# Kernel optimization log

Hardware: AMD Instinct MI355X
Metric: run time of the kernel (lower is better)

Reference implementation:

```python
import jax, jax.numpy as jnp
import numpy as np

# ---- static configuration (matches init_kwargs / input_specs) ----
B, DIM, H, W = 2, 32, 512, 512
FOLD, P, HDIM, NCLS, CV = 8, 2, 96, 16, 96
S = P * P                      # superpixels per tile
h, w = H // FOLD, W // FOLD    # 64, 64 tile size
N = h * w                      # pixels per tile

# ---- static SSN neighbor tables (init label map -> 9 candidate spixels) ----
_lab = np.repeat(np.repeat(np.arange(S).reshape(P, P), h // P, 0), w // P, 1).reshape(-1)
_sy, _sx = _lab // P, _lab % P
_dy = np.repeat(np.array([-1, 0, 1]), 3)[:, None]
_dx = np.tile(np.array([-1, 0, 1]), 3)[:, None]
_ny, _nx = _sy[None] + _dy, _sx[None] + _dx
_valid = (_ny >= 0) & (_ny < P) & (_nx >= 0) & (_nx < P)
NBR = jnp.asarray(np.where(_valid, _ny * P + _nx, 0), dtype=jnp.int32)  # [9,N]
VALID = jnp.asarray(_valid)                                             # [9,N]

def _conv1x1(x, Wk, bk):
    return jnp.einsum('oc,bchw->bohw', Wk, x) + bk[None, :, None, None]

def _tiles(t):  # 'b c (f1 h) (f2 w) -> (b f1 f2) c h w'
    Bq, C = t.shape[:2]
    return t.reshape(Bq, C, FOLD, h, FOLD, w).transpose(0, 2, 4, 1, 3, 5).reshape(Bq * FOLD * FOLD, C, h, w)

def _pool(t):  # adaptive avg pool (h,w)->(P,P); returns [b,C,S]
    b, C = t.shape[:2]
    return t.reshape(b, C, P, h // P, P, w // P).mean((3, 5)).reshape(b, C, S)

def _affinity(Fp, cen):
    # Fp [b,Ctot,N], cen [b,Ctot,S]; squared-euclid dist pixel->9 neighbor spixels,
    # sparse softmax over the 9 candidates, then scatter to dense [b,S,N] affinity.
    d = (Fp * Fp).sum(1)[:, None, :] + (cen * cen).sum(1)[:, :, None] \
        - 2.0 * jnp.einsum('bcn,bcs->bsn', Fp, cen)          # [b,S,N]
    b = Fp.shape[0]
    idx = jnp.broadcast_to(NBR[None], (b, 9, N))
    d9 = jnp.where(VALID[None], jnp.take_along_axis(d, idx, axis=1), 1e16)
    aff = jax.nn.softmax(-d9, axis=1)                        # [b,9,N]
    bi = jnp.arange(b)[:, None, None]
    ni = jnp.arange(N)[None, None, :]
    return jnp.zeros((b, S, N), Fp.dtype).at[bi, idx, ni].add(jnp.where(VALID[None], aff, 0.0))

def setup_inputs():
    k = jax.random.split(jax.random.key(0), 6)
    return {
        'x': jax.random.normal(k[0], (B, DIM, H, W), jnp.float32),
        'feat': jax.random.normal(k[1], (B, CV, H, W), jnp.float32),
        'sdf_data': jax.random.normal(k[2], (B, DIM - 1, H, W), jnp.float32),
        'Wf': 0.1 * jax.random.normal(k[3], (HDIM, DIM), jnp.float32),
        'bf': jnp.zeros((HDIM,), jnp.float32),
        'Wsdf': 0.1 * jax.random.normal(k[4], (HDIM, DIM - 1), jnp.float32),
        'bsdf': jnp.zeros((HDIM,), jnp.float32),
        'gt': jax.random.randint(k[5], (B, H, W), 0, NCLS, jnp.int32),
    }

def _cluster(x, feat, sdf_data, Wf, bf, Wsdf, bsdf):
    hsi = _conv1x1(x, Wf, bf)
    sdf = _conv1x1(sdf_data, Wsdf, bsdf)
    pf = _tiles(feat).reshape(-1, CV, N)      # per-tile pixel (value) features
    df = _tiles(hsi).reshape(-1, HDIM, N)     # deep features
    sf = _tiles(sdf).reshape(-1, HDIM, N)     # sdf features
    b = pf.shape[0]
    cen_pf = _pool(pf.reshape(b, CV, h, w))
    cen_df = _pool(df.reshape(b, HDIM, h, w))
    cen_sf = _pool(sf.reshape(b, HDIM, h, w))
    value_centers = cen_pf.transpose(0, 2, 1)                # [b,S,C]
    Fall = jnp.concatenate([pf, df, sf], 1)
    # SSN iter 0: soft affinity, update pixel-feature centroids
    A0 = _affinity(Fall, jnp.concatenate([cen_pf, cen_df, cen_sf], 1))
    cen_pf = jnp.einsum('bsn,bcn->bcs', A0, pf) / (A0.sum(-1)[:, None, :] + 1e-16)
    # SSN iter 1 (last): final dense affinity; torch computes this under no_grad
    sim = jax.lax.stop_gradient(_affinity(Fall, jnp.concatenate([cen_pf, cen_df, cen_sf], 1)))
    mask = jax.nn.one_hot(jnp.argmax(sim, 1), S, axis=1, dtype=sim.dtype)   # hard argmax mask [b,S,N]
    sim = sim * mask
    out = (jnp.einsum('bsn,bnc->bsc', sim, pf.transpose(0, 2, 1)) + value_centers) \
          / (sim.sum(-1, keepdims=True) + 1.0)
    center_feat = out.reshape(B, FOLD * FOLD * S, CV)
    mask5 = mask.reshape(B, FOLD * FOLD, S, h, w)
    return center_feat, mask5

def _gen_labels(gt, mask5):
    T = FOLD * FOLD
    coef = jnp.arange(S, dtype=mask5.dtype).reshape(1, 1, S, 1, 1)
    small = (mask5 * coef).sum(2) + jnp.arange(0, T * S, S, dtype=mask5.dtype).reshape(1, T, 1, 1)
    spix_map = small.reshape(B, FOLD, FOLD, h, w).transpose(0, 1, 3, 2, 4).reshape(B, H, W)
    gt_r = gt.reshape(B, FOLD, h, FOLD, w).transpose(0, 1, 3, 2, 4).reshape(B, T, h, w) + 1
    gt_filt = (gt_r[:, :, None].astype(mask5.dtype) * mask5).reshape(B, T, S, N).astype(jnp.int32)
    count = jax.nn.one_hot(gt_filt, NCLS + 1, dtype=jnp.float32).sum(3)   # [B,T,S,NCLS+1]
    labels = count[..., 1:].transpose(0, 3, 1, 2).reshape(B, NCLS, T * S)
    return labels, spix_map

def reference(x, feat, sdf_data, Wf, bf, Wsdf, bsdf, gt):
    center_feat, mask5 = _cluster(x, feat, sdf_data, Wf, bf, Wsdf, bsdf)
    labels, spix_map = _gen_labels(gt, jax.lax.stop_gradient(mask5))
    return center_feat, labels, spix_map
```

## Files before the change

### kernel.cpp

```cpp
#include <hip/hip_runtime.h>
#include <hip/hip_bf16.h>


#define OFF_POOLX   0
#define OFF_POOLS   16384
#define OFF_CENPF0  32256
#define OFF_NUM1    114688
#define OFF_DEN1    163840
#define OFF_OUTNUM  214016
#define OFF_OUTDEN  263168
#define OFF_LABELS  263680
#define OFF_G       271872
#define ZERO_BASE   OFF_NUM1
#define ZERO_LEN    157184

#define OUT_CF 0
#define OUT_LB 49152
#define OUT_SP 57344

#define PL 262144

typedef float f32x4 __attribute__((ext_vector_type(4)));
typedef short bf16x8 __attribute__((ext_vector_type(8)));
typedef unsigned short u16x4 __attribute__((ext_vector_type(4)));

__device__ __forceinline__ unsigned short f2bf(float f) {
  return (unsigned short)(__float_as_uint(f) >> 16);
}

__global__ __launch_bounds__(256) void k_pool(const float* __restrict__ x,
    const float* __restrict__ feat, const float* __restrict__ sdf,
    float* __restrict__ ws) {
  int plane = blockIdx.x, f1 = blockIdx.y, tid = threadIdx.x;
  {
    int lb = blockIdx.y * gridDim.x + blockIdx.x;
    if (tid < 64) {
      int zi = lb * 64 + tid;
      if (zi < ZERO_LEN) ws[ZERO_BASE + zi] = 0.f;
    }
  }
  int b = plane / 159, ch = plane % 159;
  const float* src; int c, C, cls;
  if (ch < 32)      { src = x;    C = 32; c = ch;      cls = 0; }
  else if (ch < 63) { src = sdf;  C = 31; c = ch - 32; cls = 1; }
  else              { src = feat; C = 96; c = ch - 63; cls = 2; }
  const float* base = src + ((size_t)(b*C + c)*512 + f1*64)*512;
  int half = tid >> 7, col4 = tid & 127;
  const float* p0 = base + (size_t)half*512 + (size_t)col4*4;
  f32x4 v[16];
  float acc0 = 0.f, acc1 = 0.f;
  #pragma unroll
  for (int i = 0; i < 16; ++i)
    v[i] = *reinterpret_cast<const f32x4*>(p0 + (size_t)i*1024);
  #pragma unroll
  for (int i = 0; i < 16; ++i) { f32x4 t = v[i]; acc0 += t[0] + t[1] + t[2] + t[3]; }
  #pragma unroll
  for (int i = 0; i < 16; ++i)
    v[i] = *reinterpret_cast<const f32x4*>(p0 + (size_t)(16 + i)*1024);
  #pragma unroll
  for (int i = 0; i < 16; ++i) { f32x4 t = v[i]; acc1 += t[0] + t[1] + t[2] + t[3]; }
  acc0 += __shfl_xor(acc0, 1, 64); acc0 += __shfl_xor(acc0, 2, 64); acc0 += __shfl_xor(acc0, 4, 64);
  acc1 += __shfl_xor(acc1, 1, 64); acc1 += __shfl_xor(acc1, 2, 64); acc1 += __shfl_xor(acc1, 4, 64);
  __shared__ float part[32][2];
  int lane = tid & 63;
  if ((lane & 7) == 0) {
    int f2 = col4 >> 4, qx = (col4 >> 3) & 1;
    part[(f2*2 + qx)*2 + 0][half] = acc0;
    part[(f2*2 + qx)*2 + 1][half] = acc1;
  }
  __syncthreads();
  if (tid < 32) {
    float v2 = (part[tid][0] + part[tid][1]) * (1.f/1024.f);
    int f2 = tid >> 2, qx = (tid >> 1) & 1, qy = tid & 1;
    int tile = b*64 + f1*8 + f2, s = qy*2 + qx;
    float* dst;
    if (cls == 0)      dst = ws + OFF_POOLX  + (tile*32 + c)*4;
    else if (cls == 1) dst = ws + OFF_POOLS  + (tile*31 + c)*4;
    else               dst = ws + OFF_CENPF0 + (tile*96 + c)*4;
    dst[s] = v2;
  }
}

__global__ __launch_bounds__(256) void k_pass2(const float* __restrict__ x,
    const float* __restrict__ feat, const float* __restrict__ sdf,
    const float* __restrict__ Wf, const float* __restrict__ bfv,
    const float* __restrict__ Wsdf, const float* __restrict__ bsdf,
    float* __restrict__ ws) {
  int wg = blockIdx.x, tile = wg >> 2, seg = wg & 3, tid = threadIdx.x;
  int b = tile >> 6, tl = tile & 63, f1 = tl >> 3, f2 = tl & 7;
  __shared__ float s_cpf0[384];
  __shared__ float s_udf[128];
  __shared__ float s_usf[124];
  __shared__ float s_gc[4], s_n0[4];
  __shared__ __align__(16) unsigned short s_pfT[96][264];
  __shared__ __align__(16) unsigned short s_aT[16][264];
  __shared__ __align__(16) float s_part[2][8][260];
  float* scr  = reinterpret_cast<float*>(&s_pfT[0][0]);
  float* c_px = scr;
  float* c_ps = scr + 128;
  float* c_df = scr + 256;
  float* c_sf = scr + 640;
  for (int i = tid; i < 384; i += 256) s_cpf0[i] = ws[OFF_CENPF0 + tile*384 + i];
  if (tid < 128) c_px[tid] = ws[OFF_POOLX + tile*128 + tid];
  if (tid < 124) c_ps[tid] = ws[OFF_POOLS + tile*124 + tid];
  __syncthreads();
  for (int i = tid; i < 384; i += 256) {
    int c = i % 96, s = i / 96;
    float a = bfv[c];
    for (int k = 0; k < 32; ++k) a += Wf[c*32 + k] * c_px[k*4 + s];
    c_df[c*4 + s] = a;
    float a2 = bsdf[c];
    for (int k = 0; k < 31; ++k) a2 += Wsdf[c*31 + k] * c_ps[k*4 + s];
    c_sf[c*4 + s] = a2;
  }
  __syncthreads();
  if (tid < 128) {
    int s2 = tid >> 5, k = tid & 31;
    float u = 0.f;
    for (int c2 = 0; c2 < 96; ++c2) u += Wf[c2*32 + k] * c_df[c2*4 + s2];
    s_udf[tid] = u;
  } else if (tid < 252) {
    int t2 = tid - 128, s2 = t2 / 31, k = t2 % 31;
    float u = 0.f;
    for (int c2 = 0; c2 < 96; ++c2) u += Wsdf[c2*31 + k] * c_sf[c2*4 + s2];
    s_usf[t2] = u;
  } else {
    int s = tid - 252;
    float g = 0.f, n = 0.f;
    for (int c = 0; c < 96; ++c) {
      float a = c_df[c*4 + s], a2 = c_sf[c*4 + s];
      g += 2.f*(bfv[c]*a + bsdf[c]*a2) - (a*a + a2*a2);
      float cp = s_cpf0[c*4 + s];
      n += cp*cp;
    }
    s_gc[s] = g; s_n0[s] = n;
  }
  for (int i = tid; i < 16*264; i += 256) (&s_aT[0][0])[i] = 0;
  __syncthreads();
  int lane = tid & 63, wave = tid >> 6;
  int mrow = lane & 15, quad = lane >> 4;
  int q4 = lane * 4;
  f32x4 zero4 = {0.f, 0.f, 0.f, 0.f};
  f32x4 accC[6] = {zero4, zero4, zero4, zero4, zero4, zero4};
  float dden[4] = {0.f, 0.f, 0.f, 0.f};
  const float* xb = x   + (size_t)(b*32)*PL;
  const float* sb = sdf + (size_t)(b*31)*PL;
  const float* fb = feat+ (size_t)(b*96)*PL;
  for (int chunk = 0; chunk < 4; ++chunk) {
    int pq = seg*1024 + chunk*256 + q4;
    int goq = (f1*64 + (pq >> 6))*512 + f2*64 + (pq & 63);
    f32x4 dpd[4] = {zero4, zero4, zero4, zero4};
    f32x4 dpp[4] = {zero4, zero4, zero4, zero4};
    f32x4 vv[8];
    #pragma unroll
    for (int i = 0; i < 8; ++i)
      vv[i] = *reinterpret_cast<const f32x4*>(xb + (size_t)(wave + 4*i)*PL + goq);
    #pragma unroll
    for (int i = 0; i < 8; ++i) {
      int ch = wave + 4*i;
      #pragma unroll
      for (int s = 0; s < 4; ++s) dpd[s] += vv[i] * s_udf[s*32 + ch];
    }
    #pragma unroll
    for (int i = 0; i < 8; ++i)
      if (wave + 4*i < 31)
        vv[i] = *reinterpret_cast<const f32x4*>(sb + (size_t)(wave + 4*i)*PL + goq);
    #pragma unroll
    for (int i = 0; i < 8; ++i) {
      int ch = wave + 4*i;
      if (ch < 31) {
        #pragma unroll
        for (int s = 0; s < 4; ++s) dpd[s] += vv[i] * s_usf[s*31 + ch];
      }
    }
    #pragma unroll
    for (int r = 0; r < 3; ++r) {
      #pragma unroll
      for (int i = 0; i < 8; ++i)
        vv[i] = *reinterpret_cast<const f32x4*>(fb + (size_t)(wave + 4*(r*8 + i))*PL + goq);
      #pragma unroll
      for (int i = 0; i < 8; ++i) {
        int ch = wave + 4*(r*8 + i);
        u16x4 uu = { f2bf(vv[i][0]), f2bf(vv[i][1]), f2bf(vv[i][2]), f2bf(vv[i][3]) };
        *reinterpret_cast<u16x4*>(&s_pfT[ch][q4]) = uu;
        #pragma unroll
        for (int s = 0; s < 4; ++s) dpp[s] += vv[i] * s_cpf0[ch*4 + s];
      }
    }
    if (wave >= 2) {
      #pragma unroll
      for (int s = 0; s < 4; ++s) {
        *reinterpret_cast<f32x4*>(&s_part[wave-2][s][q4]) = dpd[s];
        *reinterpret_cast<f32x4*>(&s_part[wave-2][4+s][q4]) = dpp[s];
      }
    }
    __syncthreads();
    if (wave < 2) {
      #pragma unroll
      for (int s = 0; s < 4; ++s) {
        f32x4 t = *reinterpret_cast<f32x4*>(&s_part[wave][s][q4]);
        t += dpd[s];
        *reinterpret_cast<f32x4*>(&s_part[wave][s][q4]) = t;
        f32x4 t2 = *reinterpret_cast<f32x4*>(&s_part[wave][4+s][q4]);
        t2 += dpp[s];
        *reinterpret_cast<f32x4*>(&s_part[wave][4+s][q4]) = t2;
      }
    }
    __syncthreads();
    float d0 = s_part[0][0][tid] + s_part[1][0][tid];
    float d1 = s_part[0][1][tid] + s_part[1][1][tid];
    float d2 = s_part[0][2][tid] + s_part[1][2][tid];
    float d3 = s_part[0][3][tid] + s_part[1][3][tid];
    float p0 = s_part[0][4][tid] + s_part[1][4][tid];
    float p1 = s_part[0][5][tid] + s_part[1][5][tid];
    float p2 = s_part[0][6][tid] + s_part[1][6][tid];
    float p3 = s_part[0][7][tid] + s_part[1][7][tid];
    float g0 = 2.f*d0 + s_gc[0], g1 = 2.f*d1 + s_gc[1];
    float g2 = 2.f*d2 + s_gc[2], g3 = 2.f*d3 + s_gc[3];
    int p = seg*1024 + chunk*256 + tid;
    {
      f32x4 gv = {g0, g1, g2, g3};
      *reinterpret_cast<f32x4*>(ws + OFF_G + ((size_t)tile << 14) + (size_t)p*4) = gv;
    }
    float sc0 = g0 + 2.f*p0 - s_n0[0];
    float sc1 = g1 + 2.f*p1 - s_n0[1];
    float sc2 = g2 + 2.f*p2 - s_n0[2];
    float sc3 = g3 + 2.f*p3 - s_n0[3];
    float m = fmaxf(fmaxf(sc0, sc1), fmaxf(sc2, sc3));
    float e0 = expf(sc0 - m), e1 = expf(sc1 - m), e2 = expf(sc2 - m), e3 = expf(sc3 - m);
    float inv = 1.f / (e0 + e1 + e2 + e3);
    float a0 = e0*inv, a1 = e1*inv, a2 = e2*inv, a3 = e3*inv;
    s_aT[0][tid] = f2bf(a0); s_aT[1][tid] = f2bf(a1);
    s_aT[2][tid] = f2bf(a2); s_aT[3][tid] = f2bf(a3);
    dden[0] += a0; dden[1] += a1; dden[2] += a2; dden[3] += a3;
    __syncthreads();
    #pragma unroll
    for (int kk = 0; kk < 2; ++kk) {
      int k0 = (wave*2 + kk)*32 + quad*8;
      bf16x8 bfrag = *reinterpret_cast<const bf16x8*>(&s_aT[mrow][k0]);
      #pragma unroll
      for (int mt = 0; mt < 6; ++mt) {
        bf16x8 afrag = *reinterpret_cast<const bf16x8*>(&s_pfT[mt*16 + mrow][k0]);
        accC[mt] = __builtin_amdgcn_mfma_f32_16x16x32_bf16(afrag, bfrag, accC[mt], 0, 0, 0);
      }
    }
    __syncthreads();
  }
  if (mrow < 4) {
    #pragma unroll
    for (int mt = 0; mt < 6; ++mt)
      #pragma unroll
      for (int r = 0; r < 4; ++r) {
        int c = mt*16 + quad*4 + r;
        atomicAdd(&ws[OFF_NUM1 + (tile*96 + c)*4 + mrow], accC[mt][r]);
      }
  }
  for (int m2 = 1; m2 < 64; m2 <<= 1) {
    dden[0] += __shfl_xor(dden[0], m2, 64); dden[1] += __shfl_xor(dden[1], m2, 64);
    dden[2] += __shfl_xor(dden[2], m2, 64); dden[3] += __shfl_xor(dden[3], m2, 64);
  }
  if (lane == 0) {
    atomicAdd(&ws[OFF_DEN1 + tile*4 + 0], dden[0]);
    atomicAdd(&ws[OFF_DEN1 + tile*4 + 1], dden[1]);
    atomicAdd(&ws[OFF_DEN1 + tile*4 + 2], dden[2]);
    atomicAdd(&ws[OFF_DEN1 + tile*4 + 3], dden[3]);
  }
}

__global__ __launch_bounds__(256) void k_pass3(const float* __restrict__ feat,
    const int* __restrict__ gt, float* __restrict__ ws, float* __restrict__ out) {
  int wg = blockIdx.x, tile = wg >> 2, seg = wg & 3, tid = threadIdx.x;
  int b = tile >> 6, tl = tile & 63, f1 = tl >> 3, f2 = tl & 7;
  __shared__ float s_cpf1[384];
  __shared__ float s_n1[4];
  __shared__ __align__(16) unsigned short s_pfT[96][264];
  __shared__ __align__(16) unsigned short s_aT[16][264];
  __shared__ __align__(16) float s_part[2][4][260];
  __shared__ float s_hist[64];
  if (tid < 64) s_hist[tid] = 0.f;
  for (int i = tid; i < 16*264; i += 256) (&s_aT[0][0])[i] = 0;
  for (int i = tid; i < 384; i += 256) {
    float den = ws[OFF_DEN1 + tile*4 + (i & 3)];
    s_cpf1[i] = ws[OFF_NUM1 + tile*384 + i] / (den + 1e-16f);
  }
  __syncthreads();
  if (tid < 4) {
    float n = 0.f;
    for (int c = 0; c < 96; ++c) { float v = s_cpf1[c*4 + tid]; n += v*v; }
    s_n1[tid] = n;
  }
  __syncthreads();
  int lane = tid & 63, wave = tid >> 6;
  int mrow = lane & 15, quad = lane >> 4;
  int q4 = lane * 4;
  f32x4 zero4 = {0.f, 0.f, 0.f, 0.f};
  f32x4 accC[6] = {zero4, zero4, zero4, zero4, zero4, zero4};
  float oden[4] = {0.f, 0.f, 0.f, 0.f};
  const float* fb = feat + (size_t)(b*96)*PL;
  f32x4 fvA[12], fvB[12];
  f32x4 gfut; int gtfut;
  {
    int pq = seg*1024 + q4;
    int goq = (f1*64 + (pq >> 6))*512 + f2*64 + (pq & 63);
    #pragma unroll
    for (int i = 0; i < 12; ++i)
      fvA[i] = *reinterpret_cast<const f32x4*>(fb + (size_t)(wave + 4*i)*PL + goq);
    int p0i = seg*1024 + tid;
    gfut = *reinterpret_cast<const f32x4*>(ws + OFF_G + ((size_t)tile << 14) + (size_t)p0i*4);
    gtfut = gt[b*262144 + (f1*64 + (p0i >> 6))*512 + f2*64 + (p0i & 63)];
  }
  for (int chunk = 0; chunk < 4; ++chunk) {
    int pq = seg*1024 + chunk*256 + q4;
    int goq = (f1*64 + (pq >> 6))*512 + f2*64 + (pq & 63);
    int pq1 = seg*1024 + (chunk+1)*256 + q4;
    int goq1 = (f1*64 + (pq1 >> 6))*512 + f2*64 + (pq1 & 63);
    f32x4 gcur = gfut; int gtcur = gtfut;
    f32x4 dpp[4] = {zero4, zero4, zero4, zero4};
    #pragma unroll
    for (int i = 0; i < 12; ++i)
      fvB[i] = *reinterpret_cast<const f32x4*>(fb + (size_t)(wave + 4*(12 + i))*PL + goq);
    #pragma unroll
    for (int i = 0; i < 12; ++i) {
      int ch = wave + 4*i;
      u16x4 uu = { f2bf(fvA[i][0]), f2bf(fvA[i][1]), f2bf(fvA[i][2]), f2bf(fvA[i][3]) };
      *reinterpret_cast<u16x4*>(&s_pfT[ch][q4]) = uu;
      #pragma unroll
      for (int s = 0; s < 4; ++s) dpp[s] += fvA[i] * s_cpf1[ch*4 + s];
    }
    if (chunk < 3) {
      #pragma unroll
      for (int i = 0; i < 12; ++i)
        fvA[i] = *reinterpret_cast<const f32x4*>(fb + (size_t)(wave + 4*i)*PL + goq1);
      int p1i = seg*1024 + (chunk+1)*256 + tid;
      gfut = *reinterpret_cast<const f32x4*>(ws + OFF_G + ((size_t)tile << 14) + (size_t)p1i*4);
      gtfut = gt[b*262144 + (f1*64 + (p1i >> 6))*512 + f2*64 + (p1i & 63)];
    }
    #pragma unroll
    for (int i = 0; i < 12; ++i) {
      int ch = wave + 4*(12 + i);
      u16x4 uu = { f2bf(fvB[i][0]), f2bf(fvB[i][1]), f2bf(fvB[i][2]), f2bf(fvB[i][3]) };
      *reinterpret_cast<u16x4*>(&s_pfT[ch][q4]) = uu;
      #pragma unroll
      for (int s = 0; s < 4; ++s) dpp[s] += fvB[i] * s_cpf1[ch*4 + s];
    }
    if (wave >= 2) {
      #pragma unroll
      for (int s = 0; s < 4; ++s)
        *reinterpret_cast<f32x4*>(&s_part[wave-2][s][q4]) = dpp[s];
    }
    __syncthreads();
    if (wave < 2) {
      #pragma unroll
      for (int s = 0; s < 4; ++s) {
        f32x4 t = *reinterpret_cast<f32x4*>(&s_part[wave][s][q4]);
        t += dpp[s];
        *reinterpret_cast<f32x4*>(&s_part[wave][s][q4]) = t;
      }
    }
    __syncthreads();
    int p = seg*1024 + chunk*256 + tid;
    int go = (f1*64 + (p >> 6))*512 + f2*64 + (p & 63);
    float p0 = s_part[0][0][tid] + s_part[1][0][tid];
    float p1 = s_part[0][1][tid] + s_part[1][1][tid];
    float p2 = s_part[0][2][tid] + s_part[1][2][tid];
    float p3 = s_part[0][3][tid] + s_part[1][3][tid];
    float sc0 = gcur[0] + 2.f*p0 - s_n1[0];
    float sc1 = gcur[1] + 2.f*p1 - s_n1[1];
    float sc2 = gcur[2] + 2.f*p2 - s_n1[2];
    float sc3 = gcur[3] + 2.f*p3 - s_n1[3];
    int ss = 0; float best = sc0;
    if (sc1 > best) { best = sc1; ss = 1; }
    if (sc2 > best) { best = sc2; ss = 2; }
    if (sc3 > best) { best = sc3; ss = 3; }
    float se = expf(sc0-best) + expf(sc1-best) + expf(sc2-best) + expf(sc3-best);
    float sim = 1.f / se;
    unsigned short sb = f2bf(sim);
    s_aT[0][tid] = (ss == 0) ? sb : (unsigned short)0;
    s_aT[1][tid] = (ss == 1) ? sb : (unsigned short)0;
    s_aT[2][tid] = (ss == 2) ? sb : (unsigned short)0;
    s_aT[3][tid] = (ss == 3) ? sb : (unsigned short)0;
    oden[ss] += sim;
    atomicAdd(&s_hist[ss*16 + gtcur], 1.f);
    out[OUT_SP + b*262144 + go] = (float)(tl*4 + ss);
    __syncthreads();
    #pragma unroll
    for (int kk = 0; kk < 2; ++kk) {
      int k0 = (wave*2 + kk)*32 + quad*8;
      bf16x8 bfrag = *reinterpret_cast<const bf16x8*>(&s_aT[mrow][k0]);
      #pragma unroll
      for (int mt = 0; mt < 6; ++mt) {
        bf16x8 afrag = *reinterpret_cast<const bf16x8*>(&s_pfT[mt*16 + mrow][k0]);
        accC[mt] = __builtin_amdgcn_mfma_f32_16x16x32_bf16(afrag, bfrag, accC[mt], 0, 0, 0);
      }
    }
    __syncthreads();
  }
  if (mrow < 4) {
    #pragma unroll
    for (int mt = 0; mt < 6; ++mt)
      #pragma unroll
      for (int r = 0; r < 4; ++r) {
        int c = mt*16 + quad*4 + r;
        atomicAdd(&ws[OFF_OUTNUM + (tile*96 + c)*4 + mrow], accC[mt][r]);
      }
  }
  for (int m2 = 1; m2 < 64; m2 <<= 1) {
    oden[0] += __shfl_xor(oden[0], m2, 64); oden[1] += __shfl_xor(oden[1], m2, 64);
    oden[2] += __shfl_xor(oden[2], m2, 64); oden[3] += __shfl_xor(oden[3], m2, 64);
  }
  if (lane == 0) {
    atomicAdd(&ws[OFF_OUTDEN + tile*4 + 0], oden[0]);
    atomicAdd(&ws[OFF_OUTDEN + tile*4 + 1], oden[1]);
    atomicAdd(&ws[OFF_OUTDEN + tile*4 + 2], oden[2]);
    atomicAdd(&ws[OFF_OUTDEN + tile*4 + 3], oden[3]);
  }
  if (tid < 64) atomicAdd(&ws[OFF_LABELS + tile*64 + tid], s_hist[tid]);
}

__global__ __launch_bounds__(384) void k_out(const float* __restrict__ ws,
                                             float* __restrict__ out) {
  int tile = blockIdx.x, tid = threadIdx.x;
  int b = tile >> 6, tl = tile & 63;
  int c = tid % 96, s = tid / 96;
  float od = ws[OFF_OUTDEN + tile*4 + s];
  float v = (ws[OFF_OUTNUM + (tile*96 + c)*4 + s] + ws[OFF_CENPF0 + (tile*96 + c)*4 + s]) / (od + 1.f);
  out[OUT_CF + (size_t)(b*256 + tl*4 + s)*96 + c] = v;
  if (tid < 64) {
    int s2 = tid >> 4, cls = tid & 15;
    float cnt = ws[OFF_LABELS + tile*64 + tid];
    out[OUT_LB + (b*16 + cls)*256 + tl*4 + s2] = cnt;
  }
}

extern "C" void kernel_launch(void* const* d_in, const int* in_sizes, int n_in,
                              void* d_out, int out_size, void* d_ws, size_t ws_size,
                              hipStream_t stream) {
  const float* x    = (const float*)d_in[0];
  const float* feat = (const float*)d_in[1];
  const float* sdf  = (const float*)d_in[2];
  const float* Wf   = (const float*)d_in[3];
  const float* bfv  = (const float*)d_in[4];
  const float* Wsdf = (const float*)d_in[5];
  const float* bsdf = (const float*)d_in[6];
  const int* gt = (const int*)d_in[7];
  float* ws = (float*)d_ws;
  float* out = (float*)d_out;

  k_pool <<<dim3(318, 8), 256, 0, stream>>>(x, feat, sdf, ws);
  k_pass2<<<512, 256, 0, stream>>>(x, feat, sdf, Wf, bfv, Wsdf, bsdf, ws);
  k_pass3<<<512, 256, 0, stream>>>(feat, gt, ws, out);
  k_out  <<<128, 384, 0, stream>>>(ws, out);
}
```

Baseline: 499.8 us.

## Fuse pass2, pass3 and output kernels using per-tile spin barrier and last-block finalize

Merges the three post-pool kernels into one. The four workgroups of each tile meet at an atomic-counter spin barrier before the second clustering iteration, and the last workgroup to finish a tile writes the final centers and labels. The per-pixel g values are now kept in registers instead of a global scratch buffer, and gt is loaded in the first pass. This removes two launches and a global round trip, at the cost of more registers, no more prefetching of feat in the second phase, and a spin barrier that needs all four workgroups of a tile to be resident at the same time.

```diff
diff --git a/kernel.cpp b/kernel.cpp
--- a/kernel.cpp
+++ b/kernel.cpp
@@ -10,9 +10,10 @@
 #define OFF_OUTNUM  214016
 #define OFF_OUTDEN  263168
 #define OFF_LABELS  263680
-#define OFF_G       271872
+#define OFF_CNT     271872
+#define OFF_CNT2    272000
 #define ZERO_BASE   OFF_NUM1
-#define ZERO_LEN    157184
+#define ZERO_LEN    157440
 
 #define OUT_CF 0
 #define OUT_LB 49152
@@ -26,6 +27,10 @@
 
 __device__ __forceinline__ unsigned short f2bf(float f) {
   return (unsigned short)(__float_as_uint(f) >> 16);
+}
+__device__ __forceinline__ float atomload(const float* p) {
+  int v = __hip_atomic_load((const int*)p, __ATOMIC_RELAXED, __HIP_MEMORY_SCOPE_AGENT);
+  return __int_as_float(v);
 }
 
 __global__ __launch_bounds__(256) void k_pool(const float* __restrict__ x,
@@ -81,11 +86,11 @@
   }
 }
 
-__global__ __launch_bounds__(256) void k_pass2(const float* __restrict__ x,
+__global__ __launch_bounds__(256) void k_fused(const float* __restrict__ x,
     const float* __restrict__ feat, const float* __restrict__ sdf,
     const float* __restrict__ Wf, const float* __restrict__ bfv,
     const float* __restrict__ Wsdf, const float* __restrict__ bsdf,
-    float* __restrict__ ws) {
+    const int* __restrict__ gt, float* __restrict__ ws, float* __restrict__ out) {
   int wg = blockIdx.x, tile = wg >> 2, seg = wg & 3, tid = threadIdx.x;
   int b = tile >> 6, tl = tile & 63, f1 = tl >> 3, f2 = tl & 7;
   __shared__ float s_cpf0[384];
@@ -95,6 +100,10 @@
   __shared__ __align__(16) unsigned short s_pfT[96][264];
   __shared__ __align__(16) unsigned short s_aT[16][264];
   __shared__ __align__(16) float s_part[2][8][260];
+  __shared__ float s_cpf1[384];
+  __shared__ float s_n1[4];
+  __shared__ float s_hist[64];
+  __shared__ int s_last;
   float* scr  = reinterpret_cast<float*>(&s_pfT[0][0]);
   float* c_px = scr;
   float* c_ps = scr + 128;
@@ -143,9 +152,12 @@
   f32x4 zero4 = {0.f, 0.f, 0.f, 0.f};
   f32x4 accC[6] = {zero4, zero4, zero4, zero4, zero4, zero4};
   float dden[4] = {0.f, 0.f, 0.f, 0.f};
+  f32x4 gr[4];
+  int gti[4];
   const float* xb = x   + (size_t)(b*32)*PL;
   const float* sb = sdf + (size_t)(b*31)*PL;
   const float* fb = feat+ (size_t)(b*96)*PL;
+  #pragma unroll
   for (int chunk = 0; chunk < 4; ++chunk) {
     int pq = seg*1024 + chunk*256 + q4;
     int goq = (f1*64 + (pq >> 6))*512 + f2*64 + (pq & 63);
@@ -217,10 +229,11 @@
     float p3 = s_part[0][7][tid] + s_part[1][7][tid];
     float g0 = 2.f*d0 + s_gc[0], g1 = 2.f*d1 + s_gc[1];
     float g2 = 2.f*d2 + s_gc[2], g3 = 2.f*d3 + s_gc[3];
-    int p = seg*1024 + chunk*256 + tid;
+    gr[chunk][0] = g0; gr[chunk][1] = g1; gr[chunk][2] = g2; gr[chunk][3] = g3;
     {
-      f32x4 gv = {g0, g1, g2, g3};
-      *reinterpret_cast<f32x4*>(ws + OFF_G + ((size_t)tile << 14) + (size_t)p*4) = gv;
+      int p = seg*1024 + chunk*256 + tid;
+      int go = (f1*64 + (p >> 6))*512 + f2*64 + (p & 63);
+      gti[chunk] = gt[b*262144 + go];
     }
     float sc0 = g0 + 2.f*p0 - s_n0[0];
     float sc1 = g1 + 2.f*p1 - s_n0[1];
@@ -265,24 +278,22 @@
     atomicAdd(&ws[OFF_DEN1 + tile*4 + 2], dden[2]);
     atomicAdd(&ws[OFF_DEN1 + tile*4 + 3], dden[3]);
   }
-}
-
-__global__ __launch_bounds__(256) void k_pass3(const float* __restrict__ feat,
-    const int* __restrict__ gt, float* __restrict__ ws, float* __restrict__ out) {
-  int wg = blockIdx.x, tile = wg >> 2, seg = wg & 3, tid = threadIdx.x;
-  int b = tile >> 6, tl = tile & 63, f1 = tl >> 3, f2 = tl & 7;
-  __shared__ float s_cpf1[384];
-  __shared__ float s_n1[4];
-  __shared__ __align__(16) unsigned short s_pfT[96][264];
-  __shared__ __align__(16) unsigned short s_aT[16][264];
-  __shared__ __align__(16) float s_part[2][4][260];
-  __shared__ float s_hist[64];
+  __syncthreads();
+  {
+    int* cnt = (int*)(ws + OFF_CNT) + tile;
+    if (tid == 0) {
+      __threadfence();
+      atomicAdd(cnt, 1);
+      while (__hip_atomic_load(cnt, __ATOMIC_ACQUIRE, __HIP_MEMORY_SCOPE_AGENT) < 4)
+        __builtin_amdgcn_s_sleep(2);
+    }
+    __syncthreads();
+  }
+  for (int i = tid; i < 384; i += 256) {
+    float den = atomload(&ws[OFF_DEN1 + tile*4 + (i & 3)]);
+    s_cpf1[i] = atomload(&ws[OFF_NUM1 + tile*384 + i]) / (den + 1e-16f);
+  }
   if (tid < 64) s_hist[tid] = 0.f;
-  for (int i = tid; i < 16*264; i += 256) (&s_aT[0][0])[i] = 0;
-  for (int i = tid; i < 384; i += 256) {
-    float den = ws[OFF_DEN1 + tile*4 + (i & 3)];
-    s_cpf1[i] = ws[OFF_NUM1 + tile*384 + i] / (den + 1e-16f);
-  }
   __syncthreads();
   if (tid < 4) {
     float n = 0.f;
@@ -290,58 +301,27 @@
     s_n1[tid] = n;
   }
   __syncthreads();
-  int lane = tid & 63, wave = tid >> 6;
-  int mrow = lane & 15, quad = lane >> 4;
-  int q4 = lane * 4;
-  f32x4 zero4 = {0.f, 0.f, 0.f, 0.f};
-  f32x4 accC[6] = {zero4, zero4, zero4, zero4, zero4, zero4};
+  f32x4 accD[6] = {zero4, zero4, zero4, zero4, zero4, zero4};
   float oden[4] = {0.f, 0.f, 0.f, 0.f};
-  const float* fb = feat + (size_t)(b*96)*PL;
-  f32x4 fvA[12], fvB[12];
-  f32x4 gfut; int gtfut;
-  {
-    int pq = seg*1024 + q4;
-    int goq = (f1*64 + (pq >> 6))*512 + f2*64 + (pq & 63);
-    #pragma unroll
-    for (int i = 0; i < 12; ++i)
-      fvA[i] = *reinterpret_cast<const f32x4*>(fb + (size_t)(wave + 4*i)*PL + goq);
-    int p0i = seg*1024 + tid;
-    gfut = *reinterpret_cast<const f32x4*>(ws + OFF_G + ((size_t)tile << 14) + (size_t)p0i*4);
-    gtfut = gt[b*262144 + (f1*64 + (p0i >> 6))*512 + f2*64 + (p0i & 63)];
-  }
+  #pragma unroll
   for (int chunk = 0; chunk < 4; ++chunk) {
     int pq = seg*1024 + chunk*256 + q4;
     int goq = (f1*64 + (pq >> 6))*512 + f2*64 + (pq & 63);
-    int pq1 = seg*1024 + (chunk+1)*256 + q4;
-    int goq1 = (f1*64 + (pq1 >> 6))*512 + f2*64 + (pq1 & 63);
-    f32x4 gcur = gfut; int gtcur = gtfut;
     f32x4 dpp[4] = {zero4, zero4, zero4, zero4};
-    #pragma unroll
-    for (int i = 0; i < 12; ++i)
-      fvB[i] = *reinterpret_cast<const f32x4*>(fb + (size_t)(wave + 4*(12 + i))*PL + goq);
-    #pragma unroll
-    for (int i = 0; i < 12; ++i) {
-      int ch = wave + 4*i;
-      u16x4 uu = { f2bf(fvA[i][0]), f2bf(fvA[i][1]), f2bf(fvA[i][2]), f2bf(fvA[i][3]) };
-      *reinterpret_cast<u16x4*>(&s_pfT[ch][q4]) = uu;
-      #pragma unroll
-      for (int s = 0; s < 4; ++s) dpp[s] += fvA[i] * s_cpf1[ch*4 + s];
-    }
-    if (chunk < 3) {
-      #pragma unroll
-      for (int i = 0; i < 12; ++i)
-        fvA[i] = *reinterpret_cast<const f32x4*>(fb + (size_t)(wave + 4*i)*PL + goq1);
-      int p1i = seg*1024 + (chunk+1)*256 + tid;
-      gfut = *reinterpret_cast<const f32x4*>(ws + OFF_G + ((size_t)tile << 14) + (size_t)p1i*4);
-      gtfut = gt[b*262144 + (f1*64 + (p1i >> 6))*512 + f2*64 + (p1i & 63)];
-    }
-    #pragma unroll
-    for (int i = 0; i < 12; ++i) {
-      int ch = wave + 4*(12 + i);
-      u16x4 uu = { f2bf(fvB[i][0]), f2bf(fvB[i][1]), f2bf(fvB[i][2]), f2bf(fvB[i][3]) };
-      *reinterpret_cast<u16x4*>(&s_pfT[ch][q4]) = uu;
-      #pragma unroll
-      for (int s = 0; s < 4; ++s) dpp[s] += fvB[i] * s_cpf1[ch*4 + s];
+    f32x4 vv[8];
+    #pragma unroll
+    for (int r = 0; r < 3; ++r) {
+      #pragma unroll
+      for (int i = 0; i < 8; ++i)
+        vv[i] = *reinterpret_cast<const f32x4*>(fb + (size_t)(wave + 4*(r*8 + i))*PL + goq);
+      #pragma unroll
+      for (int i = 0; i < 8; ++i) {
+        int ch = wave + 4*(r*8 + i);
+        u16x4 uu = { f2bf(vv[i][0]), f2bf(vv[i][1]), f2bf(vv[i][2]), f2bf(vv[i][3]) };
+        *reinterpret_cast<u16x4*>(&s_pfT[ch][q4]) = uu;
+        #pragma unroll
+        for (int s = 0; s < 4; ++s) dpp[s] += vv[i] * s_cpf1[ch*4 + s];
+      }
     }
     if (wave >= 2) {
       #pragma unroll
@@ -364,10 +344,10 @@
     float p1 = s_part[0][1][tid] + s_part[1][1][tid];
     float p2 = s_part[0][2][tid] + s_part[1][2][tid];
     float p3 = s_part[0][3][tid] + s_part[1][3][tid];
-    float sc0 = gcur[0] + 2.f*p0 - s_n1[0];
-    float sc1 = gcur[1] + 2.f*p1 - s_n1[1];
-    float sc2 = gcur[2] + 2.f*p2 - s_n1[2];
-    float sc3 = gcur[3] + 2.f*p3 - s_n1[3];
+    float sc0 = gr[chunk][0] + 2.f*p0 - s_n1[0];
+    float sc1 = gr[chunk][1] + 2.f*p1 - s_n1[1];
+    float sc2 = gr[chunk][2] + 2.f*p2 - s_n1[2];
+    float sc3 = gr[chunk][3] + 2.f*p3 - s_n1[3];
     int ss = 0; float best = sc0;
     if (sc1 > best) { best = sc1; ss = 1; }
     if (sc2 > best) { best = sc2; ss = 2; }
@@ -380,7 +360,7 @@
     s_aT[2][tid] = (ss == 2) ? sb : (unsigned short)0;
     s_aT[3][tid] = (ss == 3) ? sb : (unsigned short)0;
     oden[ss] += sim;
-    atomicAdd(&s_hist[ss*16 + gtcur], 1.f);
+    atomicAdd(&s_hist[ss*16 + gti[chunk]], 1.f);
     out[OUT_SP + b*262144 + go] = (float)(tl*4 + ss);
     __syncthreads();
     #pragma unroll
@@ -390,7 +370,7 @@
       #pragma unroll
       for (int mt = 0; mt < 6; ++mt) {
         bf16x8 afrag = *reinterpret_cast<const bf16x8*>(&s_pfT[mt*16 + mrow][k0]);
-        accC[mt] = __builtin_amdgcn_mfma_f32_16x16x32_bf16(afrag, bfrag, accC[mt], 0, 0, 0);
+        accD[mt] = __builtin_amdgcn_mfma_f32_16x16x32_bf16(afrag, bfrag, accD[mt], 0, 0, 0);
       }
     }
     __syncthreads();
@@ -401,7 +381,7 @@
       #pragma unroll
       for (int r = 0; r < 4; ++r) {
         int c = mt*16 + quad*4 + r;
-        atomicAdd(&ws[OFF_OUTNUM + (tile*96 + c)*4 + mrow], accC[mt][r]);
+        atomicAdd(&ws[OFF_OUTNUM + (tile*96 + c)*4 + mrow], accD[mt][r]);
       }
   }
   for (int m2 = 1; m2 < 64; m2 <<= 1) {
@@ -415,20 +395,27 @@
     atomicAdd(&ws[OFF_OUTDEN + tile*4 + 3], oden[3]);
   }
   if (tid < 64) atomicAdd(&ws[OFF_LABELS + tile*64 + tid], s_hist[tid]);
-}
-
-__global__ __launch_bounds__(384) void k_out(const float* __restrict__ ws,
-                                             float* __restrict__ out) {
-  int tile = blockIdx.x, tid = threadIdx.x;
-  int b = tile >> 6, tl = tile & 63;
-  int c = tid % 96, s = tid / 96;
-  float od = ws[OFF_OUTDEN + tile*4 + s];
-  float v = (ws[OFF_OUTNUM + (tile*96 + c)*4 + s] + ws[OFF_CENPF0 + (tile*96 + c)*4 + s]) / (od + 1.f);
-  out[OUT_CF + (size_t)(b*256 + tl*4 + s)*96 + c] = v;
-  if (tid < 64) {
-    int s2 = tid >> 4, cls = tid & 15;
-    float cnt = ws[OFF_LABELS + tile*64 + tid];
-    out[OUT_LB + (b*16 + cls)*256 + tl*4 + s2] = cnt;
+  __syncthreads();
+  {
+    int* cnt2 = (int*)(ws + OFF_CNT2) + tile;
+    if (tid == 0) {
+      __threadfence();
+      s_last = atomicAdd(cnt2, 1);
+    }
+    __syncthreads();
+  }
+  if (s_last == 3) {
+    for (int i = tid; i < 384; i += 256) {
+      int c = i % 96, s = i / 96;
+      float od = atomload(&ws[OFF_OUTDEN + tile*4 + s]);
+      float v = (atomload(&ws[OFF_OUTNUM + (tile*96 + c)*4 + s]) +
+                 ws[OFF_CENPF0 + (tile*96 + c)*4 + s]) / (od + 1.f);
+      out[OUT_CF + (size_t)(b*256 + tl*4 + s)*96 + c] = v;
+    }
+    if (tid < 64) {
+      int s2 = tid >> 4, cls = tid & 15;
+      out[OUT_LB + (b*16 + cls)*256 + tl*4 + s2] = atomload(&ws[OFF_LABELS + tile*64 + tid]);
+    }
   }
 }
 
@@ -447,7 +434,5 @@
   float* out = (float*)d_out;
 
   k_pool <<<dim3(318, 8), 256, 0, stream>>>(x, feat, sdf, ws);
-  k_pass2<<<512, 256, 0, stream>>>(x, feat, sdf, Wf, bfv, Wsdf, bsdf, ws);
-  k_pass3<<<512, 256, 0, stream>>>(feat, gt, ws, out);
-  k_out  <<<128, 384, 0, stream>>>(ws, out);
+  k_fused<<<512, 256, 0, stream>>>(x, feat, sdf, Wf, bfv, Wsdf, bsdf, gt, ws, out);
 }
```

New measurement: 543.3 us. 1.09x slower.
